# Kernel optimization log

Measured on AMD Instinct MI355X. Metric: run time of the kernel, lower is better.

Reference implementation:

```python
import jax, jax.numpy as jnp
import numpy as np

HEADS = 16
HIDDEN = 1024
HEAD_DIM = HIDDEN // HEADS


def setup_inputs() -> dict:
    key = jax.random.key(0)
    ks = jax.random.split(key, 12)
    B, S, H = 2, 2048, HIDDEN
    scale = 1.0 / np.sqrt(H)
    inp = {
        'q': jax.random.normal(ks[0], (B, S, H), jnp.float32),
        'k': jax.random.normal(ks[1], (B, S, H), jnp.float32),
        'v': jax.random.normal(ks[2], (B, S, H), jnp.float32),
        'mask': jnp.ones((B, S), jnp.int32),
        'Wq': jax.random.normal(ks[3], (H, H), jnp.float32) * scale,
        'bq': jnp.zeros((H,), jnp.float32),
        'Wk': jax.random.normal(ks[4], (H, H), jnp.float32) * scale,
        'bk': jnp.zeros((H,), jnp.float32),
        'Wv': jax.random.normal(ks[5], (H, H), jnp.float32) * scale,
        'bv': jnp.zeros((H,), jnp.float32),
        'Wo': jax.random.normal(ks[6], (H, H), jnp.float32) * scale,
        'bo': jnp.zeros((H,), jnp.float32),
    }
    return inp


def reference(q, k, v, mask, Wq, bq, Wk, bk, Wv, bv, Wo, bo):
    B, S, H = q.shape
    hd = HEAD_DIM
    # projections (torch Linear: x @ W.T + b) -> [B, heads, S, hd]
    qh = (q @ Wq.T + bq).reshape(B, S, HEADS, hd).transpose(0, 2, 1, 3)
    kh = (k @ Wk.T + bk).reshape(B, S, HEADS, hd).transpose(0, 2, 1, 3)
    vh = (v @ Wv.T + bv).reshape(B, S, HEADS, hd).transpose(0, 2, 1, 3)
    # full score matrix [B, heads, Sq, Sk]
    scores = jnp.einsum('bhqd,bhkd->bhqk', qh, kh) / np.sqrt(hd)
    # mask [B, Sq] -> [B, 1, Sq, 1], masks entire query rows where mask==0
    m = mask[:, None, :, None]
    scores = jnp.where(m == 0, jnp.float32(-1e9), scores)
    attn = jax.nn.softmax(scores, axis=-1)
    # dropout omitted (eval mode / deterministic)
    y = jnp.einsum('bhqk,bhkd->bhqd', attn, vh)
    y = y.transpose(0, 2, 1, 3).reshape(B, S, H)
    return y @ Wo.T + bo
```

## Files before the change

### kernel.cpp

```cpp
#include <hip/hip_runtime.h>
#include <hip/hip_bf16.h>
#include <cstdint>

#define EL 1048576ull

typedef __bf16 bf16_t;
typedef bf16_t bf16x8 __attribute__((ext_vector_type(8)));
typedef float  f32x4  __attribute__((ext_vector_type(4)));
typedef unsigned int u32x2 __attribute__((ext_vector_type(2)));
typedef unsigned int u32x4 __attribute__((ext_vector_type(4)));

__device__ __forceinline__ unsigned short f2bf(float f) {
  unsigned int u = __builtin_bit_cast(unsigned int, f);
  u += 0x7FFFu + ((u >> 16) & 1u);
  return (unsigned short)(u >> 16);
}

__device__ __forceinline__ unsigned int cvtpk(float lo, float hi2) {
  unsigned int r;
  asm("v_cvt_pk_bf16_f32 %0, %1, %2" : "=v"(r) : "v"(lo), "v"(hi2));
  return r;
}

__device__ __forceinline__ float fexp2(float x) {
#if __has_builtin(__builtin_amdgcn_exp2f)
  return __builtin_amdgcn_exp2f(x);
#else
  return exp2f(x);
#endif
}

typedef __attribute__((address_space(1))) void as1_void;
typedef __attribute__((address_space(3))) void as3_void;
__device__ __forceinline__ void load_lds16(const void* g, void* l) {
  __builtin_amdgcn_global_load_lds((as1_void*)g, (as3_void*)l, 16, 0, 0);
}

__device__ __forceinline__ bf16x8 repack_af(const f32x4 s0v, const f32x4 s1v) {
  unsigned int c00 = cvtpk(s0v[0], s0v[1]);
  unsigned int c01 = cvtpk(s0v[2], s0v[3]);
  unsigned int c10 = cvtpk(s1v[0], s1v[1]);
  unsigned int c11 = cvtpk(s1v[2], s1v[3]);
  asm("v_permlane32_swap_b32 %0, %1" : "+v"(c00), "+v"(c10));
  asm("v_permlane16_swap_b32 %0, %1" : "+v"(c00), "+v"(c10));
  asm("v_permlane32_swap_b32 %0, %1" : "+v"(c01), "+v"(c11));
  asm("v_permlane16_swap_b32 %0, %1" : "+v"(c01), "+v"(c11));
  u32x4 wd; wd[0] = c00; wd[1] = c01; wd[2] = c10; wd[3] = c11;
  return __builtin_bit_cast(bf16x8, wd);
}

__global__ __launch_bounds__(256) void convert_all(
    const float* __restrict__ q, const float* __restrict__ k, const float* __restrict__ v,
    const float* __restrict__ wq, const float* __restrict__ wk,
    const float* __restrict__ wv, const float* __restrict__ wo,
    unsigned short* __restrict__ ws)
{
  const size_t total_v4 = 4 * EL;
  for (size_t v4 = (size_t)blockIdx.x * blockDim.x + threadIdx.x; v4 < total_v4;
       v4 += (size_t)gridDim.x * blockDim.x) {
    size_t e = v4 * 4;
    unsigned seg = (unsigned)(e >> 20);
    const float* s; size_t base;
    if      (seg < 4)   { s = q;  base = 0; }
    else if (seg < 8)   { s = k;  base = 4*EL; }
    else if (seg < 12)  { s = v;  base = 8*EL; }
    else if (seg == 12) { s = wq; base = 12*EL; }
    else if (seg == 13) { s = wk; base = 13*EL; }
    else if (seg == 14) { s = wv; base = 14*EL; }
    else                { s = wo; base = 15*EL; }
    const float4 f = *(const float4*)(s + (e - base));
    ushort4 o;
    o.x = f2bf(f.x); o.y = f2bf(f.y); o.z = f2bf(f.z); o.w = f2bf(f.w);
    size_t dst = (seg == 15) ? (e + 13 * EL) : e;
    *(ushort4*)(ws + dst) = o;
  }
}

template <int BM, int BN, int WM, int WN>
__device__ __forceinline__ void gemm_bt_main(
    const unsigned short* __restrict__ A,
    const unsigned short* __restrict__ B,
    f32x4 (&acc)[BM / WM / 16][BN / WN / 16])
{
  constexpr int K = 1024, BK = 64;
  constexpr int AM = BM / WM / 16, AN = BN / WN / 16;
  __shared__ unsigned short sA[BM * BK];
  __shared__ unsigned short sB[BN * BK];
  const int tid  = threadIdx.x;
  const int wave = tid >> 6, lane = tid & 63;
  const int wm = wave / WN, wn = wave % WN;
  const int tm = blockIdx.y * BM, tn = blockIdx.x * BN;
  const int l16 = lane & 15, hi = lane >> 4, swz = l16 & 7;

  for (int k0 = 0; k0 < K; k0 += BK) {
    __syncthreads();
#pragma unroll
    for (int i = 0; i < BM * 8 / 256; i++) {
      int p = i * 256 + tid;
      int row = p >> 3, c = p & 7;
      load_lds16(A + (size_t)(tm + row) * K + k0 + ((c ^ (row & 7)) * 8),
                 &sA[(i * 256 + wave * 64) * 8]);
    }
#pragma unroll
    for (int i = 0; i < BN * 8 / 256; i++) {
      int p = i * 256 + tid;
      int row = p >> 3, c = p & 7;
      load_lds16(B + (size_t)(tn + row) * K + k0 + ((c ^ (row & 7)) * 8),
                 &sB[(i * 256 + wave * 64) * 8]);
    }
    __syncthreads();

#pragma unroll
    for (int kk = 0; kk < 2; kk++) {
      bf16x8 af[AM], bfr[AN];
#pragma unroll
      for (int i = 0; i < AM; i++) {
        int row = wm * (BM / WM) + i * 16 + l16;
        af[i] = *(const bf16x8*)&sA[row * BK + (((kk * 4 + hi) ^ swz) * 8)];
      }
#pragma unroll
      for (int j = 0; j < AN; j++) {
        int row = wn * (BN / WN) + j * 16 + l16;
        bfr[j] = *(const bf16x8*)&sB[row * BK + (((kk * 4 + hi) ^ swz) * 8)];
      }
#pragma unroll
      for (int i = 0; i < AM; i++)
#pragma unroll
        for (int j = 0; j < AN; j++)
          acc[i][j] = __builtin_amdgcn_mfma_f32_16x16x32_bf16(af[i], bfr[j], acc[i][j], 0, 0, 0);
    }
  }
}

__global__ __launch_bounds__(256, 3) void qkv_gemm(
    const unsigned short* qb, const unsigned short* kb, const unsigned short* vb,
    const unsigned short* wqb, const unsigned short* wkb, const unsigned short* wvb,
    const float* bq, const float* bk, const float* bv,
    unsigned short* Qp, unsigned short* Kp, unsigned short* Vt)
{
  const unsigned short* A; const unsigned short* B; const float* bias;
  if (blockIdx.z == 0)      { A = qb; B = wqb; bias = bq; }
  else if (blockIdx.z == 1) { A = kb; B = wkb; bias = bk; }
  else                      { A = vb; B = wvb; bias = bv; }

  f32x4 acc[4][4] = {};
  gemm_bt_main<128, 128, 2, 2>(A, B, acc);

  const int tid = threadIdx.x, wave = tid >> 6, lane = tid & 63;
  const int wm = wave >> 1, wn = wave & 1;
  const int tm = blockIdx.y * 128, tn = blockIdx.x * 128;
  const int l16 = lane & 15, hi = lane >> 4;

  if (blockIdx.z < 2) {
    unsigned short* C = (blockIdx.z == 0) ? Qp : Kp;
    const float scale = (blockIdx.z == 0) ? 0.18033688011112042f : 1.0f;
#pragma unroll
    for (int i = 0; i < 4; i++) {
      int row0 = tm + wm * 64 + i * 16 + hi * 4;
#pragma unroll
      for (int j = 0; j < 4; j++) {
        int col = tn + wn * 64 + j * 16 + l16;
        float bv2 = bias[col];
#pragma unroll
        for (int r = 0; r < 4; r++)
          C[(size_t)(row0 + r) * 1024 + col] = f2bf((acc[i][j][r] + bv2) * scale);
      }
    }
  } else {
#pragma unroll
    for (int i = 0; i < 4; i++) {
      int row0 = tm + wm * 64 + i * 16 + hi * 4;
      int bb = row0 >> 11, s = row0 & 2047;
#pragma unroll
      for (int j = 0; j < 4; j++) {
        int col = tn + wn * 64 + j * 16 + l16;
        int hh = col >> 6, d = col & 63;
        float bv2 = bias[col];
        u32x2 w;
        w[0] = cvtpk(acc[i][j][0] + bv2, acc[i][j][1] + bv2);
        w[1] = cvtpk(acc[i][j][2] + bv2, acc[i][j][3] + bv2);
        *(u32x2*)&Vt[((size_t)(bb * 16 + hh) * 64 + d) * 2048 + s] = w;
      }
    }
  }
}

__global__ __launch_bounds__(256, 2) void out_gemm(
    const unsigned short* Yb, const unsigned short* wob, const float* bo, float* out)
{
  f32x4 acc[2][4] = {};
  gemm_bt_main<128, 64, 4, 1>(Yb, wob, acc);

  const int tid = threadIdx.x, wave = tid >> 6, lane = tid & 63;
  const int tm = blockIdx.y * 128, tn = blockIdx.x * 64;
  const int l16 = lane & 15, hi = lane >> 4;
#pragma unroll
  for (int i = 0; i < 2; i++) {
    int row0 = tm + wave * 32 + i * 16 + hi * 4;
#pragma unroll
    for (int j = 0; j < 4; j++) {
      int col = tn + j * 16 + l16;
      float bv2 = bo[col];
#pragma unroll
      for (int r = 0; r < 4; r++)
        out[(size_t)(row0 + r) * 1024 + col] = acc[i][j][r] + bv2;
    }
  }
}

__global__ __launch_bounds__(512, 4) void attn_kernel(
    const unsigned short* __restrict__ Qp, const unsigned short* __restrict__ Kp,
    const unsigned short* __restrict__ Vt, const int* __restrict__ mask,
    float* __restrict__ O0, float* __restrict__ O1,
    float* __restrict__ l0, float* __restrict__ l1)
{
  constexpr int S = 2048, H = 1024;
  __shared__ unsigned short sK[2][128 * 64];
  __shared__ unsigned short sV[2][64 * 128];

  const int tid = threadIdx.x, wave = tid >> 6, lane = tid & 63;
  const int l16 = lane & 15, hi = lane >> 4, swz = l16 & 7;
  const int qt = blockIdx.x * 256;
  const int h = blockIdx.y;
  const int b = blockIdx.z >> 1, half = blockIdx.z & 1;
  const int bh = b * 16 + h;
  const unsigned short* Qb = Qp + (size_t)b * S * H + (size_t)h * 64;
  const unsigned short* Kb = Kp + (size_t)b * S * H + (size_t)h * 64;
  const unsigned short* Vb = Vt + (size_t)bh * 64 * 2048;

  const int kinv0 = l16 * 64 + ((hi ^ swz) * 8);
  const int kinv1 = l16 * 64 + (((4 + hi) ^ swz) * 8);
  const int vinv0 = l16 * 128 + ((hi ^ swz) * 8);
  const int vinv1 = l16 * 128 + (((4 + hi) ^ swz) * 8);

  unsigned short* sQ = &sK[0][0];
#pragma unroll
  for (int i = 0; i < 4; i++) {
    int p = i * 512 + tid, row = p >> 3, c = p & 7;
    load_lds16(Qb + (size_t)(qt + row) * H + ((c ^ (row & 7)) * 8),
               &sQ[(i * 512 + wave * 64) * 8]);
  }
  asm volatile("s_waitcnt vmcnt(0)" ::: "memory");
  __builtin_amdgcn_sched_barrier(0);
  __builtin_amdgcn_s_barrier();

  bf16x8 qf[2][2];
#pragma unroll
  for (int m = 0; m < 2; m++) {
    const int row = wave * 32 + m * 16 + l16;
    const int qm = mask[(size_t)b * S + qt + row];
#pragma unroll
    for (int ks = 0; ks < 2; ks++) {
      bf16x8 v = *(const bf16x8*)&sQ[row * 64 + (((ks * 4 + hi) ^ swz) * 8)];
      u32x4 u = __builtin_bit_cast(u32x4, v);
#pragma unroll
      for (int c = 0; c < 4; c++) u[c] = qm ? u[c] : 0u;
      qf[m][ks] = __builtin_bit_cast(bf16x8, u);
    }
  }
  __syncthreads();

  const unsigned short* pK0; const unsigned short* pK1;
  const unsigned short* pV0; const unsigned short* pV1;
  {
    int row = tid >> 3, c = tid & 7;
    int cs = (c ^ (row & 7)) * 8;
    pK0 = Kb + (size_t)(half * 1024 + row) * H + cs;
    pK1 = Kb + (size_t)(half * 1024 + 64 + row) * H + cs;
    int d = tid >> 4, kvc = tid & 15;
    int sg = ((kvc ^ d) & 7) | (kvc & 8);
    pV0 = Vb + (size_t)d * 2048 + half * 1024 + sg * 8;
    pV1 = Vb + (size_t)(32 + d) * 2048 + half * 1024 + sg * 8;
  }

  load_lds16(pK0, &sK[0][(wave * 64) * 8]);
  load_lds16(pK1, &sK[0][(512 + wave * 64) * 8]);
  load_lds16(pV0, &sV[0][(wave * 64) * 8]);
  load_lds16(pV1, &sV[0][(512 + wave * 64) * 8]);
  pK0 += 128 * H; pK1 += 128 * H; pV0 += 128; pV1 += 128;

  float lsum[2] = {0.f, 0.f};
  f32x4 oacc[2][4] = {};

  for (int t = 0; t < 8; t++) {
    const int cur = t & 1;
    if (t < 7) {
      unsigned short* nK = sK[cur ^ 1];
      unsigned short* nV = sV[cur ^ 1];
      load_lds16(pK0, &nK[(wave * 64) * 8]);
      load_lds16(pK1, &nK[(512 + wave * 64) * 8]);
      load_lds16(pV0, &nV[(wave * 64) * 8]);
      load_lds16(pV1, &nV[(512 + wave * 64) * 8]);
      pK0 += 128 * H; pK1 += 128 * H; pV0 += 128; pV1 += 128;
      asm volatile("s_waitcnt vmcnt(4)" ::: "memory");
    } else {
      asm volatile("s_waitcnt vmcnt(0)" ::: "memory");
    }
    __builtin_amdgcn_sched_barrier(0);
    __builtin_amdgcn_s_barrier();

    const unsigned short* kb = sK[cur];
    const unsigned short* vb = sV[cur];

#pragma unroll
    for (int hf = 0; hf < 2; hf++) {
      f32x4 sf[2][4];
      __builtin_amdgcn_s_setprio(1);
#pragma unroll
      for (int jj = 0; jj < 4; jj++) {
        const int ro = (hf * 4 + jj) * 1024;
        bf16x8 kf0 = *(const bf16x8*)&kb[ro + kinv0];
        bf16x8 kf1 = *(const bf16x8*)&kb[ro + kinv1];
#pragma unroll
        for (int m = 0; m < 2; m++) {
          f32x4 acc = {};
          acc = __builtin_amdgcn_mfma_f32_16x16x32_bf16(kf0, qf[m][0], acc, 0, 0, 0);
          acc = __builtin_amdgcn_mfma_f32_16x16x32_bf16(kf1, qf[m][1], acc, 0, 0, 0);
          sf[m][jj] = acc;
        }
      }
      __builtin_amdgcn_s_setprio(0);

#pragma unroll
      for (int m = 0; m < 2; m++) {
#pragma unroll
        for (int jj = 0; jj < 4; jj++)
#pragma unroll
          for (int r = 0; r < 4; r++)
            sf[m][jj][r] = fexp2(sf[m][jj][r] - 16.0f);
        f32x4 c4 = (sf[m][0] + sf[m][1]) + (sf[m][2] + sf[m][3]);
        lsum[m] += (c4[0] + c4[1]) + (c4[2] + c4[3]);
      }

#pragma unroll
      for (int w2 = 0; w2 < 2; w2++) {
        bf16x8 af0 = repack_af(sf[0][2 * w2], sf[0][2 * w2 + 1]);
        bf16x8 af1 = repack_af(sf[1][2 * w2], sf[1][2 * w2 + 1]);
        const int gw = hf * 2 + w2;
        const int vo = ((gw & 2) ? 64 : 0) + ((gw & 1) ? vinv1 : vinv0);
        __builtin_amdgcn_s_setprio(1);
#pragma unroll
        for (int n = 0; n < 4; n++) {
          bf16x8 vf = *(const bf16x8*)&vb[n * 2048 + vo];
          oacc[0][n] = __builtin_amdgcn_mfma_f32_16x16x32_bf16(af0, vf, oacc[0][n], 0, 0, 0);
          oacc[1][n] = __builtin_amdgcn_mfma_f32_16x16x32_bf16(af1, vf, oacc[1][n], 0, 0, 0);
        }
        __builtin_amdgcn_s_setprio(0);
      }
    }
    __builtin_amdgcn_sched_barrier(0);
    __builtin_amdgcn_s_barrier();
  }

  float* Op = half ? O1 : O0;
  float* lp = half ? l1 : l0;
#pragma unroll
  for (int m = 0; m < 2; m++) {
    lsum[m] += __shfl_xor(lsum[m], 16);
    lsum[m] += __shfl_xor(lsum[m], 32);
    if (hi == 0)
      lp[((size_t)b * S + qt + wave * 32 + m * 16 + l16) * 16 + h] = lsum[m];
#pragma unroll
    for (int n = 0; n < 4; n++)
#pragma unroll
      for (int r = 0; r < 4; r++) {
        int row = qt + wave * 32 + m * 16 + hi * 4 + r;
        int col = n * 16 + l16;
        Op[((size_t)b * S + row) * 1024 + h * 64 + col] = oacc[m][n][r];
      }
  }
}

__global__ __launch_bounds__(256) void combine_kernel(
    const float* __restrict__ O0, const float* __restrict__ O1,
    const float* __restrict__ l0, const float* __restrict__ l1,
    unsigned short* __restrict__ Yb)
{
  size_t idx = (size_t)blockIdx.x * 256 + threadIdx.x;
  size_t e = idx * 8;
  int row = (int)(e >> 10), hh = (int)((e >> 6) & 15);
  float l = l0[row * 16 + hh] + l1[row * 16 + hh];
  float rl = 1.0f / l;
  f32x4 a0 = *(const f32x4*)(O0 + e), a1 = *(const f32x4*)(O0 + e + 4);
  f32x4 b0 = *(const f32x4*)(O1 + e), b1 = *(const f32x4*)(O1 + e + 4);
  u32x4 w;
  w[0] = cvtpk((a0[0] + b0[0]) * rl, (a0[1] + b0[1]) * rl);
  w[1] = cvtpk((a0[2] + b0[2]) * rl, (a0[3] + b0[3]) * rl);
  w[2] = cvtpk((a1[0] + b1[0]) * rl, (a1[1] + b1[1]) * rl);
  w[3] = cvtpk((a1[2] + b1[2]) * rl, (a1[3] + b1[3]) * rl);
  *(u32x4*)(Yb + e) = w;
}

extern "C" void kernel_launch(void* const* d_in, const int* in_sizes, int n_in,
                              void* d_out, int out_size, void* d_ws, size_t ws_size,
                              hipStream_t stream)
{
  const float* q  = (const float*)d_in[0];
  const float* k  = (const float*)d_in[1];
  const float* v  = (const float*)d_in[2];
  const int*  mask = (const int*)d_in[3];
  const float* Wq = (const float*)d_in[4];
  const float* bq = (const float*)d_in[5];
  const float* Wk = (const float*)d_in[6];
  const float* bk = (const float*)d_in[7];
  const float* Wv = (const float*)d_in[8];
  const float* bv = (const float*)d_in[9];
  const float* Wo = (const float*)d_in[10];
  const float* bo = (const float*)d_in[11];

  unsigned short* ws  = (unsigned short*)d_ws;
  unsigned short* qb  = ws;
  unsigned short* kb  = ws + 4 * EL;
  unsigned short* vb  = ws + 8 * EL;
  unsigned short* wqb = ws + 12 * EL;
  unsigned short* wkb = ws + 13 * EL;
  unsigned short* wvb = ws + 14 * EL;
  unsigned short* wob = ws + 28 * EL;
  unsigned short* Qp  = ws + 16 * EL;
  unsigned short* Kp  = ws + 20 * EL;
  unsigned short* Vt  = ws + 24 * EL;
  float* O0 = (float*)ws;
  float* O1 = (float*)(ws + 8 * EL);
  float* l0 = (float*)(ws + 29 * EL);
  float* l1 = l0 + 65536;
  unsigned short* Yb  = ws + 16 * EL;

  convert_all<<<2048, 256, 0, stream>>>(q, k, v, Wq, Wk, Wv, Wo, ws);
  qkv_gemm<<<dim3(8, 32, 3), 256, 0, stream>>>(qb, kb, vb, wqb, wkb, wvb,
                                               bq, bk, bv, Qp, Kp, Vt);
  attn_kernel<<<dim3(8, 16, 4), 512, 0, stream>>>(Qp, Kp, Vt, mask, O0, O1, l0, l1);
  combine_kernel<<<2048, 256, 0, stream>>>(O0, O1, l0, l1, Yb);
  out_gemm<<<dim3(16, 32), 256, 0, stream>>>(Yb, wob, bo, (float*)d_out);
}
```

Baseline: 125.9 us.

## Fuse activation conversion into QKV GEMM and drop split-KV attention combine

The QKV GEMM now loads fp32 activations directly and converts them to bf16 while staging into LDS, so the standalone conversion pass only handles weights. Attention stops splitting the key range into two halves: each block walks all 16 KV tiles and writes normalized bf16 output directly, which removes the fp32 partial buffers and the combine kernel. The cost is that the GEMM A-tile load becomes register-staged instead of async global-to-LDS and doubles its global read bytes. Attention also launches half as many blocks, each with twice the serial work, which reduces parallelism.

```diff
diff --git a/kernel.cpp b/kernel.cpp
--- a/kernel.cpp
+++ b/kernel.cpp
@@ -49,43 +49,33 @@
   return __builtin_bit_cast(bf16x8, wd);
 }
 
-__global__ __launch_bounds__(256) void convert_all(
-    const float* __restrict__ q, const float* __restrict__ k, const float* __restrict__ v,
+__global__ __launch_bounds__(256) void convert_w(
     const float* __restrict__ wq, const float* __restrict__ wk,
     const float* __restrict__ wv, const float* __restrict__ wo,
     unsigned short* __restrict__ ws)
 {
-  const size_t total_v4 = 4 * EL;
-  for (size_t v4 = (size_t)blockIdx.x * blockDim.x + threadIdx.x; v4 < total_v4;
+  for (size_t v4 = (size_t)blockIdx.x * blockDim.x + threadIdx.x; v4 < EL;
        v4 += (size_t)gridDim.x * blockDim.x) {
     size_t e = v4 * 4;
     unsigned seg = (unsigned)(e >> 20);
-    const float* s; size_t base;
-    if      (seg < 4)   { s = q;  base = 0; }
-    else if (seg < 8)   { s = k;  base = 4*EL; }
-    else if (seg < 12)  { s = v;  base = 8*EL; }
-    else if (seg == 12) { s = wq; base = 12*EL; }
-    else if (seg == 13) { s = wk; base = 13*EL; }
-    else if (seg == 14) { s = wv; base = 14*EL; }
-    else                { s = wo; base = 15*EL; }
-    const float4 f = *(const float4*)(s + (e - base));
+    const float* s = (seg == 0) ? wq : (seg == 1) ? wk : (seg == 2) ? wv : wo;
+    const float4 f = *(const float4*)(s + (e & (EL - 1)));
     ushort4 o;
     o.x = f2bf(f.x); o.y = f2bf(f.y); o.z = f2bf(f.z); o.w = f2bf(f.w);
-    size_t dst = (seg == 15) ? (e + 13 * EL) : e;
-    *(ushort4*)(ws + dst) = o;
-  }
-}
-
-template <int BM, int BN, int WM, int WN>
+    *(ushort4*)(ws + e) = o;
+  }
+}
+
+template <int BM, int BN, int WM, int WN, bool AF32>
 __device__ __forceinline__ void gemm_bt_main(
-    const unsigned short* __restrict__ A,
+    const void* __restrict__ A,
     const unsigned short* __restrict__ B,
     f32x4 (&acc)[BM / WM / 16][BN / WN / 16])
 {
   constexpr int K = 1024, BK = 64;
   constexpr int AM = BM / WM / 16, AN = BN / WN / 16;
-  __shared__ unsigned short sA[BM * BK];
-  __shared__ unsigned short sB[BN * BK];
+  __shared__ __align__(16) unsigned short sA[BM * BK];
+  __shared__ __align__(16) unsigned short sB[BN * BK];
   const int tid  = threadIdx.x;
   const int wave = tid >> 6, lane = tid & 63;
   const int wm = wave / WN, wn = wave % WN;
@@ -94,12 +84,29 @@
 
   for (int k0 = 0; k0 < K; k0 += BK) {
     __syncthreads();
-#pragma unroll
-    for (int i = 0; i < BM * 8 / 256; i++) {
-      int p = i * 256 + tid;
-      int row = p >> 3, c = p & 7;
-      load_lds16(A + (size_t)(tm + row) * K + k0 + ((c ^ (row & 7)) * 8),
-                 &sA[(i * 256 + wave * 64) * 8]);
+    if constexpr (AF32) {
+      const float* Af = (const float*)A;
+#pragma unroll
+      for (int i = 0; i < BM * 8 / 256; i++) {
+        int p = i * 256 + tid;
+        int row = p >> 3, c = p & 7;
+        const float* src = Af + (size_t)(tm + row) * K + k0 + ((c ^ (row & 7)) * 8);
+        float4 f0 = *(const float4*)src;
+        float4 f1 = *(const float4*)(src + 4);
+        u32x4 w;
+        w[0] = cvtpk(f0.x, f0.y); w[1] = cvtpk(f0.z, f0.w);
+        w[2] = cvtpk(f1.x, f1.y); w[3] = cvtpk(f1.z, f1.w);
+        *(u32x4*)&sA[(size_t)p * 8] = w;
+      }
+    } else {
+      const unsigned short* Ab = (const unsigned short*)A;
+#pragma unroll
+      for (int i = 0; i < BM * 8 / 256; i++) {
+        int p = i * 256 + tid;
+        int row = p >> 3, c = p & 7;
+        load_lds16(Ab + (size_t)(tm + row) * K + k0 + ((c ^ (row & 7)) * 8),
+                   &sA[(i * 256 + wave * 64) * 8]);
+      }
     }
 #pragma unroll
     for (int i = 0; i < BN * 8 / 256; i++) {
@@ -133,18 +140,18 @@
 }
 
 __global__ __launch_bounds__(256, 3) void qkv_gemm(
-    const unsigned short* qb, const unsigned short* kb, const unsigned short* vb,
+    const float* q, const float* k, const float* v,
     const unsigned short* wqb, const unsigned short* wkb, const unsigned short* wvb,
     const float* bq, const float* bk, const float* bv,
     unsigned short* Qp, unsigned short* Kp, unsigned short* Vt)
 {
-  const unsigned short* A; const unsigned short* B; const float* bias;
-  if (blockIdx.z == 0)      { A = qb; B = wqb; bias = bq; }
-  else if (blockIdx.z == 1) { A = kb; B = wkb; bias = bk; }
-  else                      { A = vb; B = wvb; bias = bv; }
+  const float* A; const unsigned short* B; const float* bias;
+  if (blockIdx.z == 0)      { A = q; B = wqb; bias = bq; }
+  else if (blockIdx.z == 1) { A = k; B = wkb; bias = bk; }
+  else                      { A = v; B = wvb; bias = bv; }
 
   f32x4 acc[4][4] = {};
-  gemm_bt_main<128, 128, 2, 2>(A, B, acc);
+  gemm_bt_main<128, 128, 2, 2, true>(A, B, acc);
 
   const int tid = threadIdx.x, wave = tid >> 6, lane = tid & 63;
   const int wm = wave >> 1, wn = wave & 1;
@@ -189,7 +196,7 @@
     const unsigned short* Yb, const unsigned short* wob, const float* bo, float* out)
 {
   f32x4 acc[2][4] = {};
-  gemm_bt_main<128, 64, 4, 1>(Yb, wob, acc);
+  gemm_bt_main<128, 64, 4, 1, false>(Yb, wob, acc);
 
   const int tid = threadIdx.x, wave = tid >> 6, lane = tid & 63;
   const int tm = blockIdx.y * 128, tn = blockIdx.x * 64;
@@ -211,19 +218,16 @@
 __global__ __launch_bounds__(512, 4) void attn_kernel(
     const unsigned short* __restrict__ Qp, const unsigned short* __restrict__ Kp,
     const unsigned short* __restrict__ Vt, const int* __restrict__ mask,
-    float* __restrict__ O0, float* __restrict__ O1,
-    float* __restrict__ l0, float* __restrict__ l1)
+    unsigned short* __restrict__ Yb)
 {
   constexpr int S = 2048, H = 1024;
-  __shared__ unsigned short sK[2][128 * 64];
-  __shared__ unsigned short sV[2][64 * 128];
+  __shared__ __align__(16) unsigned short sK[2][128 * 64];
+  __shared__ __align__(16) unsigned short sV[2][64 * 128];
 
   const int tid = threadIdx.x, wave = tid >> 6, lane = tid & 63;
   const int l16 = lane & 15, hi = lane >> 4, swz = l16 & 7;
   const int qt = blockIdx.x * 256;
-  const int h = blockIdx.y;
-  const int b = blockIdx.z >> 1, half = blockIdx.z & 1;
-  const int bh = b * 16 + h;
+  const int h = blockIdx.y, b = blockIdx.z, bh = b * 16 + h;
   const unsigned short* Qb = Qp + (size_t)b * S * H + (size_t)h * 64;
   const unsigned short* Kb = Kp + (size_t)b * S * H + (size_t)h * 64;
   const unsigned short* Vb = Vt + (size_t)bh * 64 * 2048;
@@ -265,12 +269,12 @@
   {
     int row = tid >> 3, c = tid & 7;
     int cs = (c ^ (row & 7)) * 8;
-    pK0 = Kb + (size_t)(half * 1024 + row) * H + cs;
-    pK1 = Kb + (size_t)(half * 1024 + 64 + row) * H + cs;
+    pK0 = Kb + (size_t)row * H + cs;
+    pK1 = Kb + (size_t)(64 + row) * H + cs;
     int d = tid >> 4, kvc = tid & 15;
     int sg = ((kvc ^ d) & 7) | (kvc & 8);
-    pV0 = Vb + (size_t)d * 2048 + half * 1024 + sg * 8;
-    pV1 = Vb + (size_t)(32 + d) * 2048 + half * 1024 + sg * 8;
+    pV0 = Vb + (size_t)d * 2048 + sg * 8;
+    pV1 = Vb + (size_t)(32 + d) * 2048 + sg * 8;
   }
 
   load_lds16(pK0, &sK[0][(wave * 64) * 8]);
@@ -282,9 +286,9 @@
   float lsum[2] = {0.f, 0.f};
   f32x4 oacc[2][4] = {};
 
-  for (int t = 0; t < 8; t++) {
+  for (int t = 0; t < 16; t++) {
     const int cur = t & 1;
-    if (t < 7) {
+    if (t < 15) {
       unsigned short* nK = sK[cur ^ 1];
       unsigned short* nV = sV[cur ^ 1];
       load_lds16(pK0, &nK[(wave * 64) * 8]);
@@ -352,43 +356,25 @@
     __builtin_amdgcn_s_barrier();
   }
 
-  float* Op = half ? O1 : O0;
-  float* lp = half ? l1 : l0;
 #pragma unroll
   for (int m = 0; m < 2; m++) {
     lsum[m] += __shfl_xor(lsum[m], 16);
     lsum[m] += __shfl_xor(lsum[m], 32);
-    if (hi == 0)
-      lp[((size_t)b * S + qt + wave * 32 + m * 16 + l16) * 16 + h] = lsum[m];
+  }
+#pragma unroll
+  for (int m = 0; m < 2; m++) {
+    float lr[4];
+#pragma unroll
+    for (int r = 0; r < 4; r++) lr[r] = 1.0f / __shfl(lsum[m], hi * 4 + r);
 #pragma unroll
     for (int n = 0; n < 4; n++)
 #pragma unroll
       for (int r = 0; r < 4; r++) {
         int row = qt + wave * 32 + m * 16 + hi * 4 + r;
         int col = n * 16 + l16;
-        Op[((size_t)b * S + row) * 1024 + h * 64 + col] = oacc[m][n][r];
-      }
-  }
-}
-
-__global__ __launch_bounds__(256) void combine_kernel(
-    const float* __restrict__ O0, const float* __restrict__ O1,
-    const float* __restrict__ l0, const float* __restrict__ l1,
-    unsigned short* __restrict__ Yb)
-{
-  size_t idx = (size_t)blockIdx.x * 256 + threadIdx.x;
-  size_t e = idx * 8;
-  int row = (int)(e >> 10), hh = (int)((e >> 6) & 15);
-  float l = l0[row * 16 + hh] + l1[row * 16 + hh];
-  float rl = 1.0f / l;
-  f32x4 a0 = *(const f32x4*)(O0 + e), a1 = *(const f32x4*)(O0 + e + 4);
-  f32x4 b0 = *(const f32x4*)(O1 + e), b1 = *(const f32x4*)(O1 + e + 4);
-  u32x4 w;
-  w[0] = cvtpk((a0[0] + b0[0]) * rl, (a0[1] + b0[1]) * rl);
-  w[1] = cvtpk((a0[2] + b0[2]) * rl, (a0[3] + b0[3]) * rl);
-  w[2] = cvtpk((a1[0] + b1[0]) * rl, (a1[1] + b1[1]) * rl);
-  w[3] = cvtpk((a1[2] + b1[2]) * rl, (a1[3] + b1[3]) * rl);
-  *(u32x4*)(Yb + e) = w;
+        Yb[((size_t)b * S + row) * H + h * 64 + col] = f2bf(oacc[m][n][r] * lr[r]);
+      }
+  }
 }
 
 extern "C" void kernel_launch(void* const* d_in, const int* in_sizes, int n_in,
@@ -409,26 +395,18 @@
   const float* bo = (const float*)d_in[11];
 
   unsigned short* ws  = (unsigned short*)d_ws;
-  unsigned short* qb  = ws;
-  unsigned short* kb  = ws + 4 * EL;
-  unsigned short* vb  = ws + 8 * EL;
-  unsigned short* wqb = ws + 12 * EL;
-  unsigned short* wkb = ws + 13 * EL;
-  unsigned short* wvb = ws + 14 * EL;
-  unsigned short* wob = ws + 28 * EL;
-  unsigned short* Qp  = ws + 16 * EL;
-  unsigned short* Kp  = ws + 20 * EL;
-  unsigned short* Vt  = ws + 24 * EL;
-  float* O0 = (float*)ws;
-  float* O1 = (float*)(ws + 8 * EL);
-  float* l0 = (float*)(ws + 29 * EL);
-  float* l1 = l0 + 65536;
+  unsigned short* wqb = ws;
+  unsigned short* wkb = ws + 1 * EL;
+  unsigned short* wvb = ws + 2 * EL;
+  unsigned short* wob = ws + 3 * EL;
+  unsigned short* Qp  = ws + 4 * EL;
+  unsigned short* Kp  = ws + 8 * EL;
+  unsigned short* Vt  = ws + 12 * EL;
   unsigned short* Yb  = ws + 16 * EL;
 
-  convert_all<<<2048, 256, 0, stream>>>(q, k, v, Wq, Wk, Wv, Wo, ws);
-  qkv_gemm<<<dim3(8, 32, 3), 256, 0, stream>>>(qb, kb, vb, wqb, wkb, wvb,
+  convert_w<<<1024, 256, 0, stream>>>(Wq, Wk, Wv, Wo, ws);
+  qkv_gemm<<<dim3(8, 32, 3), 256, 0, stream>>>(q, k, v, wqb, wkb, wvb,
                                                bq, bk, bv, Qp, Kp, Vt);
-  attn_kernel<<<dim3(8, 16, 4), 512, 0, stream>>>(Qp, Kp, Vt, mask, O0, O1, l0, l1);
-  combine_kernel<<<2048, 256, 0, stream>>>(O0, O1, l0, l1, Yb);
+  attn_kernel<<<dim3(8, 16, 2), 512, 0, stream>>>(Qp, Kp, Vt, mask, Yb);
   out_gemm<<<dim3(16, 32), 256, 0, stream>>>(Yb, wob, bo, (float*)d_out);
 }
```

Result: slower. 142.1 us (+12.9%).
